# Kernel optimization log

Hardware: AMD Instinct MI355X
Metric: run time of the kernel (lower is better)

Reference implementation:

```python
import jax, jax.numpy as jnp
import numpy as np

N = 50000
NEG_SLOPE_ATT = 0.2    # PyG GATConv attention leaky_relu slope
NEG_SLOPE_ACT = 0.01   # torch F.leaky_relu default slope


def leaky(x, s):
    return jnp.where(x >= 0, x, s * x)


def gat_conv(x, src, dst, W, att_src, att_dst, bias):
    """PyG GATConv (concat=True, dropout off, self-loops already in src/dst).
    x: [N, F_in]; W: [F_in, H*C]; att_src/att_dst: [H, C]; bias: [H*C]."""
    H, C = att_src.shape
    h = (x @ W).reshape(N, H, C)                       # [N, H, C]
    a_src = (h * att_src[None]).sum(-1)                # [N, H]
    a_dst = (h * att_dst[None]).sum(-1)                # [N, H]
    e = leaky(a_src[src] + a_dst[dst], NEG_SLOPE_ATT)  # [E, H]
    # numerically-stable softmax over incoming edges of each dst node
    m = jax.ops.segment_max(e, dst, num_segments=N)    # [N, H]
    ex = jnp.exp(e - m[dst])
    Z = jax.ops.segment_sum(ex, dst, num_segments=N)   # [N, H]
    alpha = ex / (Z[dst] + 1e-16)                      # [E, H]
    msg = h[src] * alpha[:, :, None]                   # [E, H, C]
    out = jax.ops.segment_sum(msg, dst, num_segments=N)
    return out.reshape(N, H * C) + bias[None, :]


def setup_inputs() -> dict:
    key = jax.random.key(0)
    ks = jax.random.split(key, 12)
    E = 800000
    in_c, hid, heads, out_c = 256, 32, 4, 128
    hc = hid * heads  # 128
    x = jax.random.normal(ks[0], (N, in_c), dtype=jnp.float32)
    edge_index = jax.random.randint(ks[1], (2, E), 0, N, dtype=jnp.int64)
    s1 = 1.0 / np.sqrt(in_c)
    s2 = 1.0 / np.sqrt(hc)
    return {
        "x": x,
        "edge_index": edge_index,
        "W1": jax.random.normal(ks[2], (in_c, heads * hid), dtype=jnp.float32) * s1,
        "att_src1": jax.random.normal(ks[3], (heads, hid), dtype=jnp.float32) * s2,
        "att_dst1": jax.random.normal(ks[4], (heads, hid), dtype=jnp.float32) * s2,
        "b1": jnp.zeros((hc,), dtype=jnp.float32),
        "W2": jax.random.normal(ks[5], (hc, out_c), dtype=jnp.float32) * s2,
        "att_src2": jax.random.normal(ks[6], (1, out_c), dtype=jnp.float32) * s2,
        "att_dst2": jax.random.normal(ks[7], (1, out_c), dtype=jnp.float32) * s2,
        "b2": jnp.zeros((out_c,), dtype=jnp.float32),
    }


def reference(x, edge_index, W1, att_src1, att_dst1, b1, W2, att_src2, att_dst2, b2):
    # add self loops (PyG GATConv default add_self_loops=True)
    loops = jnp.arange(N, dtype=edge_index.dtype)
    src = jnp.concatenate([edge_index[0], loops])
    dst = jnp.concatenate([edge_index[1], loops])
    h = leaky(gat_conv(x, src, dst, W1, att_src1, att_dst1, b1), NEG_SLOPE_ACT)
    out = leaky(gat_conv(h, src, dst, W2, att_src2, att_dst2, b2), NEG_SLOPE_ACT)
    return out
```

## Files before the change

kernel.cpp:

```cpp
#include <hip/hip_runtime.h>
#include <hip/hip_fp16.h>

#define SLOPE_ATT 0.2f
#define SLOPE_ACT 0.01f

#define NB_CSR 128
#define CHUNK 8192

typedef _Float16 hf8 __attribute__((ext_vector_type(8)));
typedef float f32x4 __attribute__((ext_vector_type(4)));

template<int K, int H, bool A_FP32>
__device__ __forceinline__
void gemm_mfma_body(int gbid, int tid,
                    const void* __restrict__ Av, const _Float16* __restrict__ BT,
                    const float* __restrict__ att_s, const float* __restrict__ att_d,
                    _Float16* __restrict__ hout, float* __restrict__ a_src,
                    float* __restrict__ a_dst, int M)
{
  const int lane = tid & 63;
  const int wid  = tid >> 6;
  const int li   = lane & 15;
  const int lk   = lane >> 4;
  const int rowbase = gbid * 128 + wid * 32;

  const float*    Af = (const float*)Av;
  const _Float16* Ah = (const _Float16*)Av;

  f32x4 acc[2][8];
#pragma unroll
  for (int i = 0; i < 2; ++i)
#pragma unroll
    for (int j = 0; j < 8; ++j) acc[i][j] = (f32x4){0.f, 0.f, 0.f, 0.f};

  const int r0 = min(rowbase + li,      M - 1);
  const int r1 = min(rowbase + 16 + li, M - 1);

#pragma unroll
  for (int ks = 0; ks < K / 32; ++ks) {
    const int kb = ks * 32 + lk * 8;
    hf8 a0, a1;
    if constexpr (A_FP32) {
      const float* p0 = &Af[(size_t)r0 * K + kb];
      const float* p1 = &Af[(size_t)r1 * K + kb];
      float4 x0a = *(const float4*)p0, x0b = *(const float4*)(p0 + 4);
      float4 x1a = *(const float4*)p1, x1b = *(const float4*)(p1 + 4);
      a0[0]=(_Float16)x0a.x; a0[1]=(_Float16)x0a.y; a0[2]=(_Float16)x0a.z; a0[3]=(_Float16)x0a.w;
      a0[4]=(_Float16)x0b.x; a0[5]=(_Float16)x0b.y; a0[6]=(_Float16)x0b.z; a0[7]=(_Float16)x0b.w;
      a1[0]=(_Float16)x1a.x; a1[1]=(_Float16)x1a.y; a1[2]=(_Float16)x1a.z; a1[3]=(_Float16)x1a.w;
      a1[4]=(_Float16)x1b.x; a1[5]=(_Float16)x1b.y; a1[6]=(_Float16)x1b.z; a1[7]=(_Float16)x1b.w;
    } else {
      a0 = *(const hf8*)&Ah[(size_t)r0 * K + kb];
      a1 = *(const hf8*)&Ah[(size_t)r1 * K + kb];
    }
#pragma unroll
    for (int cf = 0; cf < 8; ++cf) {
      hf8 b = *(const hf8*)&BT[(size_t)(cf * 16 + li) * K + kb];
      acc[0][cf] = __builtin_amdgcn_mfma_f32_16x16x32_f16(a0, b, acc[0][cf], 0, 0, 0);
      acc[1][cf] = __builtin_amdgcn_mfma_f32_16x16x32_f16(a1, b, acc[1][cf], 0, 0, 0);
    }
  }

  float sA[8], dA[8];
#pragma unroll
  for (int cf = 0; cf < 8; ++cf) {
    sA[cf] = att_s[cf * 16 + li];
    dA[cf] = att_d[cf * 16 + li];
  }

  const bool full = (rowbase + 32) <= M;
#pragma unroll
  for (int rf = 0; rf < 2; ++rf) {
    const int rb = rowbase + rf * 16 + lk * 4;
#pragma unroll
    for (int reg = 0; reg < 4; ++reg) {
      const int r = rb + reg;
      if (full || r < M) {
#pragma unroll
        for (int cf = 0; cf < 8; ++cf)
          hout[(size_t)r * 128 + cf * 16 + li] = (_Float16)acc[rf][cf][reg];
      }
    }
    if constexpr (H == 4) {
#pragma unroll
      for (int hh = 0; hh < 4; ++hh) {
#pragma unroll
        for (int reg = 0; reg < 4; ++reg) {
          float sp = acc[rf][2*hh][reg] * sA[2*hh] + acc[rf][2*hh+1][reg] * sA[2*hh+1];
          float dp = acc[rf][2*hh][reg] * dA[2*hh] + acc[rf][2*hh+1][reg] * dA[2*hh+1];
          sp += __shfl_xor(sp, 1); sp += __shfl_xor(sp, 2);
          sp += __shfl_xor(sp, 4); sp += __shfl_xor(sp, 8);
          dp += __shfl_xor(dp, 1); dp += __shfl_xor(dp, 2);
          dp += __shfl_xor(dp, 4); dp += __shfl_xor(dp, 8);
          const int r = rb + reg;
          if (li == 0 && r < M) {
            a_src[(size_t)r * 4 + hh] = sp;
            a_dst[(size_t)r * 4 + hh] = dp;
          }
        }
      }
    } else {
#pragma unroll
      for (int reg = 0; reg < 4; ++reg) {
        float sp = 0.f, dp = 0.f;
#pragma unroll
        for (int cf = 0; cf < 8; ++cf) {
          sp += acc[rf][cf][reg] * sA[cf];
          dp += acc[rf][cf][reg] * dA[cf];
        }
        sp += __shfl_xor(sp, 1); sp += __shfl_xor(sp, 2);
        sp += __shfl_xor(sp, 4); sp += __shfl_xor(sp, 8);
        dp += __shfl_xor(dp, 1); dp += __shfl_xor(dp, 2);
        dp += __shfl_xor(dp, 4); dp += __shfl_xor(dp, 8);
        const int r = rb + reg;
        if (li == 0 && r < M) { a_src[r] = sp; a_dst[r] = dp; }
      }
    }
  }
}

__global__ __launch_bounds__(256)
void fused_pre_kernel(const int* __restrict__ ei, int E, int N,
                      unsigned short* __restrict__ cnt16mat,
                      unsigned short* __restrict__ rank16,
                      unsigned* __restrict__ sd32,
                      const float* __restrict__ W1, _Float16* __restrict__ W1T,
                      const float* __restrict__ W2, _Float16* __restrict__ W2T,
                      int ncount)
{
  __shared__ unsigned cnt[CHUNK];
  const int bid = blockIdx.x;
  if (bid < ncount) {
    const int b = bid % NB_CSR;
    const int c0 = (bid / NB_CSR) * CHUNK;
    const int clen = min(CHUNK, N - c0);
    const int EE = E + N;
    const int epb = (EE + NB_CSR - 1) / NB_CSR;
    const int lo = b * epb, hi = min(lo + epb, EE);

    for (int j = threadIdx.x; j < clen; j += 256) cnt[j] = 0;
    __syncthreads();
    for (int i = lo + threadIdx.x; i < hi; i += 256) {
      int d = (i < E) ? ei[E + i] : (i - E);
      int r = d - c0;
      if (r >= 0 && r < clen) {
        unsigned rank = atomicAdd(&cnt[r], 1u);
        rank16[i] = (unsigned short)rank;
      }
    }
    __syncthreads();
    for (int j = threadIdx.x; j < clen; j += 256)
      cnt16mat[(size_t)b * N + c0 + j] = (unsigned short)cnt[j];
  } else {
    int rem = bid - ncount;
    if (rem < 128) {
      int idx = rem * 256 + threadIdx.x;
      int k = idx >> 7, c = idx & 127;
      W1T[(size_t)c * 256 + k] = (_Float16)W1[idx];
    } else if (rem < 192) {
      int idx = (rem - 128) * 256 + threadIdx.x;
      int k = idx >> 7, c = idx & 127;
      W2T[(size_t)c * 128 + k] = (_Float16)W2[idx];
    } else {
      const int i = (rem - 192) * 256 + threadIdx.x;
      const int EE = E + N;
      if (i < EE) {
        unsigned s, d;
        if (i < E) { s = (unsigned)ei[i]; d = (unsigned)ei[E + i]; }
        else       { s = d = (unsigned)(i - E); }
        sd32[i] = (s << 16) | d;
      }
    }
  }
}

__global__ __launch_bounds__(256)
void colscan_kernel(unsigned short* __restrict__ cnt16mat,
                    unsigned* __restrict__ deg, unsigned* __restrict__ bsum, int N)
{
  __shared__ unsigned red[256];
  const int d2 = blockIdx.x * 256 + threadIdx.x;
  const int N2 = N >> 1;
  unsigned off0 = 0, off1 = 0;
  if (d2 < N2) {
    unsigned* pm = (unsigned*)cnt16mat;
#pragma unroll 8
    for (int b = 0; b < NB_CSR; ++b) {
      unsigned t = pm[(size_t)b * N2 + d2];
      pm[(size_t)b * N2 + d2] = off0 | (off1 << 16);
      off0 += t & 0xFFFFu;
      off1 += t >> 16;
    }
    deg[2 * d2]     = off0;
    deg[2 * d2 + 1] = off1;
  }
  red[threadIdx.x] = off0 + off1;
  __syncthreads();
  for (int o = 128; o; o >>= 1) {
    if (threadIdx.x < o) red[threadIdx.x] += red[threadIdx.x + o];
    __syncthreads();
  }
  if (threadIdx.x == 0) bsum[blockIdx.x] = red[0];
}

__global__ __launch_bounds__(256)
void rowstart_kernel(const unsigned* __restrict__ deg, const unsigned* __restrict__ bsum,
                     unsigned* __restrict__ row_start, int N, int nblk)
{
  __shared__ unsigned s[256];
  __shared__ unsigned boff_sh;
  const int t = threadIdx.x;
  unsigned v0 = (t < nblk) ? bsum[t] : 0u;
  s[t] = v0;
  __syncthreads();
  for (int off = 1; off < 256; off <<= 1) {
    unsigned v = (t >= off) ? s[t - off] : 0u;
    __syncthreads();
    s[t] += v;
    __syncthreads();
  }
  if (t == (int)blockIdx.x) boff_sh = s[t] - v0;
  __syncthreads();
  const unsigned boff = boff_sh;
  __syncthreads();
  const int i = blockIdx.x * 512 + t * 2;
  unsigned d0 = (i < N) ? deg[i] : 0u;
  unsigned d1 = (i + 1 < N) ? deg[i + 1] : 0u;
  s[t] = d0 + d1;
  __syncthreads();
  for (int off = 1; off < 256; off <<= 1) {
    unsigned v = (t >= off) ? s[t - off] : 0u;
    __syncthreads();
    s[t] += v;
    __syncthreads();
  }
  unsigned base = boff + s[t] - (d0 + d1);
  if (i < N)     row_start[i] = base;
  if (i + 1 < N) row_start[i + 1] = base + d0;
}

__global__ __launch_bounds__(256)
void fused_mid_kernel(int E, int N, int epb,
                      const unsigned* __restrict__ sd32,
                      const unsigned short* __restrict__ cnt16mat,
                      const unsigned short* __restrict__ rank16,
                      const unsigned* __restrict__ row_start,
                      unsigned short* __restrict__ csr16,
                      const float* __restrict__ x, const _Float16* __restrict__ W1T,
                      const float* __restrict__ as1, const float* __restrict__ ad1,
                      _Float16* __restrict__ h, float* __restrict__ asv,
                      float* __restrict__ adv, int ggrid)
{
  const int bid = blockIdx.x;
  if (bid < ggrid) {
    gemm_mfma_body<256, 4, true>(bid, threadIdx.x, x, W1T, as1, ad1,
                                 h, asv, adv, N);
  } else {
    const int i = (bid - ggrid) * 256 + threadIdx.x;
    const int EE = E + N;
    if (i < EE) {
      const unsigned sd = sd32[i];
      const unsigned d = sd & 0xFFFFu;
      const int b = i / epb;
      unsigned pos = row_start[d] + cnt16mat[(size_t)b * N + d] + rank16[i];
      csr16[pos] = (unsigned short)(sd >> 16);
    }
  }
}

__global__ __launch_bounds__(256)
void agg1_gemm2_kernel(const unsigned* __restrict__ row_start,
                       const unsigned* __restrict__ deg,
                       const unsigned short* __restrict__ csr16,
                       const __half* __restrict__ h,
                       const float* __restrict__ a_src,
                       const float* __restrict__ a_dst,
                       const float* __restrict__ bias,
                       const _Float16* __restrict__ W2T,
                       const float* __restrict__ as2, const float* __restrict__ ad2,
                       _Float16* __restrict__ h2,
                       float* __restrict__ asv2, float* __restrict__ adv2, int N)
{
  __shared__ _Float16 actS[16][136];
  __shared__ float sdots[2][16];

  const int lane = threadIdx.x & 63;
  const int wid  = threadIdx.x >> 6;
  const int l5   = lane & 15;
  const int nl   = wid * 4 + (lane >> 4);
  const int nb   = blockIdx.x * 16;
  const int n    = nb + nl;
  const int nn   = min(n, N - 1);
  const int hd   = l5 >> 2;

  const float adn = a_dst[(size_t)nn * 4 + hd];
  const unsigned beg = row_start[nn];
  const unsigned cnt = deg[nn];
  unsigned cmax = cnt;
  cmax = max(cmax, (unsigned)__shfl_xor((int)cmax, 16));
  cmax = max(cmax, (unsigned)__shfl_xor((int)cmax, 32));

  const float4* __restrict__ h4 = (const float4*)h;

  float Z = 0.f;
  float acc[8];
#pragma unroll
  for (int j = 0; j < 8; ++j) acc[j] = 0.f;

  unsigned i = 0;
  for (; i + 2 <= cmax; i += 2) {
    unsigned s0 = csr16[beg + min(i,     cnt - 1)];
    unsigned s1 = csr16[beg + min(i + 1, cnt - 1)];
    float e0 = a_src[(size_t)s0 * 4 + hd] + adn;
    float e1 = a_src[(size_t)s1 * 4 + hd] + adn;
    float4 v0 = h4[(size_t)s0 * 16 + l5];
    float4 v1 = h4[(size_t)s1 * 16 + l5];
    e0 = (e0 >= 0.f) ? e0 : SLOPE_ATT * e0;
    e1 = (e1 >= 0.f) ? e1 : SLOPE_ATT * e1;
    float w0 = (i     < cnt) ? __expf(e0) : 0.f;
    float w1 = (i + 1 < cnt) ? __expf(e1) : 0.f;
    Z += w0 + w1;
    const __half2* p0 = (const __half2*)&v0;
    const __half2* p1 = (const __half2*)&v1;
#pragma unroll
    for (int j = 0; j < 4; ++j) {
      float2 f0 = __half22float2(p0[j]);
      float2 f1 = __half22float2(p1[j]);
      acc[2*j]   += w0 * f0.x + w1 * f1.x;
      acc[2*j+1] += w0 * f0.y + w1 * f1.y;
    }
  }
  if (i < cmax) {
    unsigned s0 = csr16[beg + min(i, cnt - 1)];
    float e0 = a_src[(size_t)s0 * 4 + hd] + adn;
    float4 v0 = h4[(size_t)s0 * 16 + l5];
    e0 = (e0 >= 0.f) ? e0 : SLOPE_ATT * e0;
    float w0 = (i < cnt) ? __expf(e0) : 0.f;
    Z += w0;
    const __half2* p0 = (const __half2*)&v0;
#pragma unroll
    for (int j = 0; j < 4; ++j) {
      float2 f0 = __half22float2(p0[j]);
      acc[2*j]   += w0 * f0.x;
      acc[2*j+1] += w0 * f0.y;
    }
  }

  const float inv = 1.f / (Z + 1e-16f);
  float4 b0 = ((const float4*)bias)[l5 * 2];
  float4 b1 = ((const float4*)bias)[l5 * 2 + 1];
  float o[8];
  o[0] = acc[0] * inv + b0.x;  o[1] = acc[1] * inv + b0.y;
  o[2] = acc[2] * inv + b0.z;  o[3] = acc[3] * inv + b0.w;
  o[4] = acc[4] * inv + b1.x;  o[5] = acc[5] * inv + b1.y;
  o[6] = acc[6] * inv + b1.z;  o[7] = acc[7] * inv + b1.w;
#pragma unroll
  for (int j = 0; j < 8; ++j) o[j] = (o[j] >= 0.f) ? o[j] : SLOPE_ACT * o[j];

#pragma unroll
  for (int j = 0; j < 8; ++j) actS[nl][l5 * 8 + j] = (_Float16)o[j];
  if (threadIdx.x < 32) sdots[threadIdx.x >> 4][threadIdx.x & 15] = 0.f;
  __syncthreads();

  const int li = l5;
  const int lk = lane >> 4;
#pragma unroll
  for (int t = 0; t < 2; ++t) {
    const int c0 = wid * 32 + t * 16;
    f32x4 a2 = (f32x4){0.f, 0.f, 0.f, 0.f};
#pragma unroll
    for (int ks = 0; ks < 4; ++ks) {
      hf8 af = *(const hf8*)&actS[li][ks * 32 + lk * 8];
      hf8 bf = *(const hf8*)&W2T[(size_t)(c0 + li) * 128 + ks * 32 + lk * 8];
      a2 = __builtin_amdgcn_mfma_f32_16x16x32_f16(af, bf, a2, 0, 0, 0);
    }
    const float asc = as2[c0 + li];
    const float adc = ad2[c0 + li];
#pragma unroll
    for (int reg = 0; reg < 4; ++reg) {
      const int r = lk * 4 + reg;
      float hv = a2[reg];
      if (nb + r < N) h2[(size_t)(nb + r) * 128 + c0 + li] = (_Float16)hv;
      float sp = hv * asc;
      float dp = hv * adc;
      sp += __shfl_xor(sp, 1); sp += __shfl_xor(sp, 2);
      sp += __shfl_xor(sp, 4); sp += __shfl_xor(sp, 8);
      dp += __shfl_xor(dp, 1); dp += __shfl_xor(dp, 2);
      dp += __shfl_xor(dp, 4); dp += __shfl_xor(dp, 8);
      if (li == 0) {
        atomicAdd(&sdots[0][r], sp);
        atomicAdd(&sdots[1][r], dp);
      }
    }
  }
  __syncthreads();
  if (threadIdx.x < 16) {
    const int r = threadIdx.x;
    if (nb + r < N) {
      asv2[nb + r] = sdots[0][r];
      adv2[nb + r] = sdots[1][r];
    }
  }
}

__global__ __launch_bounds__(256)
void aggregate2_kernel(const unsigned* __restrict__ row_start,
                       const unsigned* __restrict__ deg,
                       const unsigned short* __restrict__ csr16,
                       const __half* __restrict__ h,
                       const float* __restrict__ a_src,
                       const float* __restrict__ a_dst,
                       const float* __restrict__ bias,
                       float* __restrict__ out, int N)
{
  const int lane = threadIdx.x & 63;
  const int wid  = threadIdx.x >> 6;
  const int l5   = lane & 15;
  const int n    = blockIdx.x * 16 + wid * 4 + (lane >> 4);
  const int nn   = min(n, N - 1);

  const float adn = a_dst[nn];
  const unsigned beg = row_start[nn];
  const unsigned cnt = deg[nn];
  unsigned cmax = cnt;
  cmax = max(cmax, (unsigned)__shfl_xor((int)cmax, 16));
  cmax = max(cmax, (unsigned)__shfl_xor((int)cmax, 32));

  const float4* __restrict__ h4 = (const float4*)h;

  float Z = 0.f;
  float acc[8];
#pragma unroll
  for (int j = 0; j < 8; ++j) acc[j] = 0.f;

  unsigned i = 0;
  for (; i + 2 <= cmax; i += 2) {
    unsigned s0 = csr16[beg + min(i,     cnt - 1)];
    unsigned s1 = csr16[beg + min(i + 1, cnt - 1)];
    float e0 = a_src[s0] + adn;
    float e1 = a_src[s1] + adn;
    float4 v0 = h4[(size_t)s0 * 16 + l5];
    float4 v1 = h4[(size_t)s1 * 16 + l5];
    e0 = (e0 >= 0.f) ? e0 : SLOPE_ATT * e0;
    e1 = (e1 >= 0.f) ? e1 : SLOPE_ATT * e1;
    float w0 = (i     < cnt) ? __expf(e0) : 0.f;
    float w1 = (i + 1 < cnt) ? __expf(e1) : 0.f;
    Z += w0 + w1;
    const __half2* p0 = (const __half2*)&v0;
    const __half2* p1 = (const __half2*)&v1;
#pragma unroll
    for (int j = 0; j < 4; ++j) {
      float2 f0 = __half22float2(p0[j]);
      float2 f1 = __half22float2(p1[j]);
      acc[2*j]   += w0 * f0.x + w1 * f1.x;
      acc[2*j+1] += w0 * f0.y + w1 * f1.y;
    }
  }
  if (i < cmax) {
    unsigned s0 = csr16[beg + min(i, cnt - 1)];
    float e0 = a_src[s0] + adn;
    float4 v0 = h4[(size_t)s0 * 16 + l5];
    e0 = (e0 >= 0.f) ? e0 : SLOPE_ATT * e0;
    float w0 = (i < cnt) ? __expf(e0) : 0.f;
    Z += w0;
    const __half2* p0 = (const __half2*)&v0;
#pragma unroll
    for (int j = 0; j < 4; ++j) {
      float2 f0 = __half22float2(p0[j]);
      acc[2*j]   += w0 * f0.x;
      acc[2*j+1] += w0 * f0.y;
    }
  }

  const float inv = 1.f / (Z + 1e-16f);
  float4 b0 = ((const float4*)bias)[l5 * 2];
  float4 b1 = ((const float4*)bias)[l5 * 2 + 1];
  float o[8];
  o[0] = acc[0] * inv + b0.x;  o[1] = acc[1] * inv + b0.y;
  o[2] = acc[2] * inv + b0.z;  o[3] = acc[3] * inv + b0.w;
  o[4] = acc[4] * inv + b1.x;  o[5] = acc[5] * inv + b1.y;
  o[6] = acc[6] * inv + b1.z;  o[7] = acc[7] * inv + b1.w;
#pragma unroll
  for (int j = 0; j < 8; ++j) o[j] = (o[j] >= 0.f) ? o[j] : SLOPE_ACT * o[j];

  if (n < N) {
    ((float4*)out)[(size_t)n * 32 + l5 * 2]     = make_float4(o[0], o[1], o[2], o[3]);
    ((float4*)out)[(size_t)n * 32 + l5 * 2 + 1] = make_float4(o[4], o[5], o[6], o[7]);
  }
}

extern "C" void kernel_launch(void* const* d_in, const int* in_sizes, int n_in,
                              void* d_out, int out_size, void* d_ws, size_t ws_size,
                              hipStream_t stream)
{
  const float* x   = (const float*)d_in[0];
  const int*   ei  = (const int*)d_in[1];
  const float* W1  = (const float*)d_in[2];
  const float* as1 = (const float*)d_in[3];
  const float* ad1 = (const float*)d_in[4];
  const float* b1  = (const float*)d_in[5];
  const float* W2  = (const float*)d_in[6];
  const float* as2 = (const float*)d_in[7];
  const float* ad2 = (const float*)d_in[8];
  const float* b2  = (const float*)d_in[9];
  float* out = (float*)d_out;

  const int N  = in_sizes[0] / 256;
  const int E  = in_sizes[1] / 2;
  const int EE = E + N;
  const int NCH  = (N + CHUNK - 1) / CHUNK;
  const int nblk = (N + 511) / 512;
  const int NSC  = NB_CSR * NCH;
  const int epb  = (EE + NB_CSR - 1) / NB_CSR;
  const int pgrid = (EE + 255) / 256;

  float* ws = (float*)d_ws;
  size_t o = 0;
  _Float16* h    = (_Float16*)(ws + o); o += (size_t)N * 64;
  _Float16* h2   = (_Float16*)(ws + o); o += (size_t)N * 64;
  float* asv  = ws + o; o += (size_t)N * 4;
  float* adv  = ws + o; o += (size_t)N * 4;
  float* asv2 = ws + o; o += (size_t)N;
  float* adv2 = ws + o; o += (size_t)N;
  _Float16* W1T = (_Float16*)(ws + o); o += 128 * 256 / 2;
  _Float16* W2T = (_Float16*)(ws + o); o += 128 * 128 / 2;
  unsigned* deg       = (unsigned*)(ws + o); o += (size_t)N;
  unsigned* row_start = (unsigned*)(ws + o); o += (size_t)N;
  unsigned* bsum      = (unsigned*)(ws + o); o += 256;
  unsigned* sd32      = (unsigned*)(ws + o); o += (size_t)EE;
  unsigned short* csr16    = (unsigned short*)(ws + o); o += (size_t)(EE + 1) / 2;
  unsigned short* cnt16mat = (unsigned short*)(ws + o); o += (size_t)NB_CSR * N / 2;
  unsigned short* rank16   = (unsigned short*)(ws + o); o += (size_t)(EE + 1) / 2;

  const int ngrid = (N + 15) / 16;
  const int ggrid = (N + 127) / 128;
  const int sgrid = (EE + 255) / 256;

  fused_pre_kernel<<<NSC + 192 + pgrid, 256, 0, stream>>>(
      ei, E, N, cnt16mat, rank16, sd32, W1, W1T, W2, W2T, NSC);
  colscan_kernel<<<nblk, 256, 0, stream>>>(cnt16mat, deg, bsum, N);
  rowstart_kernel<<<nblk, 256, 0, stream>>>(deg, bsum, row_start, N, nblk);
  fused_mid_kernel<<<ggrid + sgrid, 256, 0, stream>>>(
      E, N, epb, sd32, cnt16mat, rank16, row_start, csr16,
      x, W1T, as1, ad1, h, asv, adv, ggrid);
  agg1_gemm2_kernel<<<ngrid, 256, 0, stream>>>(
      row_start, deg, csr16, (const __half*)h, asv, adv, b1,
      W2T, as2, ad2, h2, asv2, adv2, N);
  aggregate2_kernel<<<ngrid, 256, 0, stream>>>(
      row_start, deg, csr16, (const __half*)h2, asv2, adv2, b2, out, N);
}
```

Before: 168.7 us.

## Replace per-node count matrix CSR build with two-level bucket radix sort

Replaces the CSR construction, which used a 128×N 16-bit count matrix, a column scan and a row-start scan, with a two-pass bucket sort. Edges are first histogrammed into 128-node buckets per block, then scanned per bucket and scattered into bucket order. Each bucket is then sorted locally in shared memory to produce deg, row_start and csr16. This drops the large count-matrix traffic and the rank array, but edge order within a row is no longer deterministic because of shared-memory atomics. It also adds an extra scatter pass and repeats the bucket-start scan in every block. The aggregation kernel's shared-memory padding is also changed from 136 to 132.

```diff
diff --git a/kernel.cpp b/kernel.cpp
--- a/kernel.cpp
+++ b/kernel.cpp
@@ -4,8 +4,8 @@
 #define SLOPE_ATT 0.2f
 #define SLOPE_ACT 0.01f
 
-#define NB_CSR 128
-#define CHUNK 8192
+#define SB 256
+#define NBUKMAX 512
 
 typedef _Float16 hf8 __attribute__((ext_vector_type(8)));
 typedef float f32x4 __attribute__((ext_vector_type(4)));
@@ -120,97 +120,54 @@
 }
 
 __global__ __launch_bounds__(256)
-void fused_pre_kernel(const int* __restrict__ ei, int E, int N,
-                      unsigned short* __restrict__ cnt16mat,
-                      unsigned short* __restrict__ rank16,
-                      unsigned* __restrict__ sd32,
-                      const float* __restrict__ W1, _Float16* __restrict__ W1T,
-                      const float* __restrict__ W2, _Float16* __restrict__ W2T,
-                      int ncount)
-{
-  __shared__ unsigned cnt[CHUNK];
+void pre_kernel(const int* __restrict__ ei, int E, int N, int nbuk, int epb1,
+                unsigned* __restrict__ cntA, unsigned* __restrict__ sd32,
+                const float* __restrict__ W1, _Float16* __restrict__ W1T,
+                const float* __restrict__ W2, _Float16* __restrict__ W2T)
+{
+  __shared__ unsigned hist[NBUKMAX];
   const int bid = blockIdx.x;
-  if (bid < ncount) {
-    const int b = bid % NB_CSR;
-    const int c0 = (bid / NB_CSR) * CHUNK;
-    const int clen = min(CHUNK, N - c0);
+  const int tid = threadIdx.x;
+  if (bid < SB) {
+    for (int j = tid; j < NBUKMAX; j += 256) hist[j] = 0;
+    __syncthreads();
     const int EE = E + N;
-    const int epb = (EE + NB_CSR - 1) / NB_CSR;
-    const int lo = b * epb, hi = min(lo + epb, EE);
-
-    for (int j = threadIdx.x; j < clen; j += 256) cnt[j] = 0;
-    __syncthreads();
-    for (int i = lo + threadIdx.x; i < hi; i += 256) {
+    const int lo = bid * epb1, hi = min(lo + epb1, EE);
+    for (int i = lo + tid; i < hi; i += 256) {
       int d = (i < E) ? ei[E + i] : (i - E);
-      int r = d - c0;
-      if (r >= 0 && r < clen) {
-        unsigned rank = atomicAdd(&cnt[r], 1u);
-        rank16[i] = (unsigned short)rank;
-      }
-    }
-    __syncthreads();
-    for (int j = threadIdx.x; j < clen; j += 256)
-      cnt16mat[(size_t)b * N + c0 + j] = (unsigned short)cnt[j];
+      atomicAdd(&hist[d >> 7], 1u);
+    }
+    __syncthreads();
+    for (int j = tid; j < nbuk; j += 256)
+      cntA[(size_t)bid * NBUKMAX + j] = hist[j];
+  } else if (bid < SB + 128) {
+    int idx = (bid - SB) * 256 + tid;
+    int k = idx >> 7, c = idx & 127;
+    W1T[(size_t)c * 256 + k] = (_Float16)W1[idx];
+  } else if (bid < SB + 192) {
+    int idx = (bid - SB - 128) * 256 + tid;
+    int k = idx >> 7, c = idx & 127;
+    W2T[(size_t)c * 128 + k] = (_Float16)W2[idx];
   } else {
-    int rem = bid - ncount;
-    if (rem < 128) {
-      int idx = rem * 256 + threadIdx.x;
-      int k = idx >> 7, c = idx & 127;
-      W1T[(size_t)c * 256 + k] = (_Float16)W1[idx];
-    } else if (rem < 192) {
-      int idx = (rem - 128) * 256 + threadIdx.x;
-      int k = idx >> 7, c = idx & 127;
-      W2T[(size_t)c * 128 + k] = (_Float16)W2[idx];
-    } else {
-      const int i = (rem - 192) * 256 + threadIdx.x;
-      const int EE = E + N;
-      if (i < EE) {
-        unsigned s, d;
-        if (i < E) { s = (unsigned)ei[i]; d = (unsigned)ei[E + i]; }
-        else       { s = d = (unsigned)(i - E); }
-        sd32[i] = (s << 16) | d;
-      }
+    const int i = (bid - SB - 192) * 256 + tid;
+    const int EE = E + N;
+    if (i < EE) {
+      unsigned s, d;
+      if (i < E) { s = (unsigned)ei[i]; d = (unsigned)ei[E + i]; }
+      else       { s = d = (unsigned)(i - E); }
+      sd32[i] = (s << 16) | d;
     }
   }
 }
 
 __global__ __launch_bounds__(256)
-void colscan_kernel(unsigned short* __restrict__ cnt16mat,
-                    unsigned* __restrict__ deg, unsigned* __restrict__ bsum, int N)
-{
-  __shared__ unsigned red[256];
-  const int d2 = blockIdx.x * 256 + threadIdx.x;
-  const int N2 = N >> 1;
-  unsigned off0 = 0, off1 = 0;
-  if (d2 < N2) {
-    unsigned* pm = (unsigned*)cnt16mat;
-#pragma unroll 8
-    for (int b = 0; b < NB_CSR; ++b) {
-      unsigned t = pm[(size_t)b * N2 + d2];
-      pm[(size_t)b * N2 + d2] = off0 | (off1 << 16);
-      off0 += t & 0xFFFFu;
-      off1 += t >> 16;
-    }
-    deg[2 * d2]     = off0;
-    deg[2 * d2 + 1] = off1;
-  }
-  red[threadIdx.x] = off0 + off1;
-  __syncthreads();
-  for (int o = 128; o; o >>= 1) {
-    if (threadIdx.x < o) red[threadIdx.x] += red[threadIdx.x + o];
-    __syncthreads();
-  }
-  if (threadIdx.x == 0) bsum[blockIdx.x] = red[0];
-}
-
-__global__ __launch_bounds__(256)
-void rowstart_kernel(const unsigned* __restrict__ deg, const unsigned* __restrict__ bsum,
-                     unsigned* __restrict__ row_start, int N, int nblk)
+void bukoff_kernel(const unsigned* __restrict__ cntA, unsigned* __restrict__ blkoff,
+                   unsigned* __restrict__ buktotal)
 {
   __shared__ unsigned s[256];
-  __shared__ unsigned boff_sh;
+  const int j = blockIdx.x;
   const int t = threadIdx.x;
-  unsigned v0 = (t < nblk) ? bsum[t] : 0u;
+  unsigned v0 = cntA[(size_t)t * NBUKMAX + j];
   s[t] = v0;
   __syncthreads();
   for (int off = 1; off < 256; off <<= 1) {
@@ -219,52 +176,111 @@
     s[t] += v;
     __syncthreads();
   }
-  if (t == (int)blockIdx.x) boff_sh = s[t] - v0;
-  __syncthreads();
-  const unsigned boff = boff_sh;
-  __syncthreads();
-  const int i = blockIdx.x * 512 + t * 2;
-  unsigned d0 = (i < N) ? deg[i] : 0u;
-  unsigned d1 = (i + 1 < N) ? deg[i + 1] : 0u;
-  s[t] = d0 + d1;
+  blkoff[(size_t)t * NBUKMAX + j] = s[t] - v0;
+  if (t == 255) buktotal[j] = s[255];
+}
+
+__device__ __forceinline__
+void bukstart_scan(const unsigned* __restrict__ buktotal, int nbuk,
+                   unsigned* bt, unsigned* ps, unsigned* bs, int tid)
+{
+  for (int j = tid; j < NBUKMAX; j += 256) bt[j] = (j < nbuk) ? buktotal[j] : 0u;
+  __syncthreads();
+  unsigned pair = bt[2 * tid] + bt[2 * tid + 1];
+  ps[tid] = pair;
   __syncthreads();
   for (int off = 1; off < 256; off <<= 1) {
-    unsigned v = (t >= off) ? s[t - off] : 0u;
-    __syncthreads();
-    s[t] += v;
-    __syncthreads();
-  }
-  unsigned base = boff + s[t] - (d0 + d1);
-  if (i < N)     row_start[i] = base;
-  if (i + 1 < N) row_start[i + 1] = base + d0;
+    unsigned v = (tid >= off) ? ps[tid - off] : 0u;
+    __syncthreads();
+    ps[tid] += v;
+    __syncthreads();
+  }
+  unsigned e0 = ps[tid] - pair;
+  bs[2 * tid]     = e0;
+  bs[2 * tid + 1] = e0 + bt[2 * tid];
+  __syncthreads();
 }
 
 __global__ __launch_bounds__(256)
-void fused_mid_kernel(int E, int N, int epb,
-                      const unsigned* __restrict__ sd32,
-                      const unsigned short* __restrict__ cnt16mat,
-                      const unsigned short* __restrict__ rank16,
-                      const unsigned* __restrict__ row_start,
-                      unsigned short* __restrict__ csr16,
-                      const float* __restrict__ x, const _Float16* __restrict__ W1T,
-                      const float* __restrict__ as1, const float* __restrict__ ad1,
-                      _Float16* __restrict__ h, float* __restrict__ asv,
-                      float* __restrict__ adv, int ggrid)
-{
+void gemm1_scatter_kernel(int E, int N, int nbuk, int epb1,
+                          const unsigned* __restrict__ sd32,
+                          const unsigned* __restrict__ blkoff,
+                          const unsigned* __restrict__ buktotal,
+                          unsigned* __restrict__ ebuk,
+                          const float* __restrict__ x, const _Float16* __restrict__ W1T,
+                          const float* __restrict__ as1, const float* __restrict__ ad1,
+                          _Float16* __restrict__ h, float* __restrict__ asv,
+                          float* __restrict__ adv, int ggrid)
+{
+  __shared__ unsigned bt[NBUKMAX], bs[NBUKMAX], cur[NBUKMAX];
+  __shared__ unsigned ps[256];
   const int bid = blockIdx.x;
+  const int tid = threadIdx.x;
   if (bid < ggrid) {
-    gemm_mfma_body<256, 4, true>(bid, threadIdx.x, x, W1T, as1, ad1,
-                                 h, asv, adv, N);
+    gemm_mfma_body<256, 4, true>(bid, tid, x, W1T, as1, ad1, h, asv, adv, N);
   } else {
-    const int i = (bid - ggrid) * 256 + threadIdx.x;
+    const int sb = bid - ggrid;
+    bukstart_scan(buktotal, nbuk, bt, ps, bs, tid);
+    for (int j = tid; j < nbuk; j += 256)
+      cur[j] = bs[j] + blkoff[(size_t)sb * NBUKMAX + j];
+    __syncthreads();
     const int EE = E + N;
-    if (i < EE) {
-      const unsigned sd = sd32[i];
-      const unsigned d = sd & 0xFFFFu;
-      const int b = i / epb;
-      unsigned pos = row_start[d] + cnt16mat[(size_t)b * N + d] + rank16[i];
-      csr16[pos] = (unsigned short)(sd >> 16);
-    }
+    const int lo = sb * epb1, hi = min(lo + epb1, EE);
+    for (int i = lo + tid; i < hi; i += 256) {
+      unsigned sd = sd32[i];
+      unsigned buk = (sd & 0xFFFFu) >> 7;
+      unsigned slot = atomicAdd(&cur[buk], 1u);
+      ebuk[slot] = sd;
+    }
+  }
+}
+
+__global__ __launch_bounds__(256)
+void csr_build_kernel(int N, int nbuk,
+                      const unsigned* __restrict__ buktotal,
+                      const unsigned* __restrict__ ebuk,
+                      unsigned* __restrict__ deg, unsigned* __restrict__ row_start,
+                      unsigned short* __restrict__ csr16)
+{
+  __shared__ unsigned bt[NBUKMAX], bs[NBUKMAX];
+  __shared__ unsigned ps[256];
+  __shared__ unsigned hist[128], hs[128], cur2[128];
+  const int j = blockIdx.x;
+  const int tid = threadIdx.x;
+
+  bukstart_scan(buktotal, nbuk, bt, ps, bs, tid);
+  const unsigned estart = bs[j];
+  const unsigned ecount = bt[j];
+  const int n0 = j * 128;
+
+  if (tid < 128) hist[tid] = 0;
+  __syncthreads();
+  for (unsigned i = estart + tid; i < estart + ecount; i += 256)
+    atomicAdd(&hist[ebuk[i] & 127u], 1u);
+  __syncthreads();
+  unsigned hv = (tid < 128) ? hist[tid] : 0u;
+  if (tid < 128) hs[tid] = hv;
+  __syncthreads();
+  for (int off = 1; off < 128; off <<= 1) {
+    unsigned v = 0;
+    if (tid < 128 && tid >= off) v = hs[tid - off];
+    __syncthreads();
+    if (tid < 128) hs[tid] += v;
+    __syncthreads();
+  }
+  if (tid < 128) {
+    unsigned excl = hs[tid] - hv;
+    cur2[tid] = estart + excl;
+    if (n0 + tid < N) {
+      deg[n0 + tid] = hv;
+      row_start[n0 + tid] = estart + excl;
+    }
+  }
+  __syncthreads();
+  for (unsigned i = estart + tid; i < estart + ecount; i += 256) {
+    unsigned sd = ebuk[i];
+    unsigned slot = atomicAdd(&cur2[sd & 127u], 1u);
+    csr16[slot] = (unsigned short)(sd >> 16);
   }
 }
 
@@ -281,7 +297,7 @@
                        _Float16* __restrict__ h2,
                        float* __restrict__ asv2, float* __restrict__ adv2, int N)
 {
-  __shared__ _Float16 actS[16][136];
+  __shared__ _Float16 actS[16][132];
   __shared__ float sdots[2][16];
 
   const int lane = threadIdx.x & 63;
@@ -508,10 +524,8 @@
   const int N  = in_sizes[0] / 256;
   const int E  = in_sizes[1] / 2;
   const int EE = E + N;
-  const int NCH  = (N + CHUNK - 1) / CHUNK;
-  const int nblk = (N + 511) / 512;
-  const int NSC  = NB_CSR * NCH;
-  const int epb  = (EE + NB_CSR - 1) / NB_CSR;
+  const int nbuk = (N + 127) / 128;
+  const int epb1 = (EE + SB - 1) / SB;
   const int pgrid = (EE + 255) / 256;
 
   float* ws = (float*)d_ws;
@@ -526,23 +540,24 @@
   _Float16* W2T = (_Float16*)(ws + o); o += 128 * 128 / 2;
   unsigned* deg       = (unsigned*)(ws + o); o += (size_t)N;
   unsigned* row_start = (unsigned*)(ws + o); o += (size_t)N;
-  unsigned* bsum      = (unsigned*)(ws + o); o += 256;
+  unsigned* cntA      = (unsigned*)(ws + o); o += (size_t)SB * NBUKMAX;
+  unsigned* blkoff    = (unsigned*)(ws + o); o += (size_t)SB * NBUKMAX;
+  unsigned* buktotal  = (unsigned*)(ws + o); o += NBUKMAX;
   unsigned* sd32      = (unsigned*)(ws + o); o += (size_t)EE;
-  unsigned short* csr16    = (unsigned short*)(ws + o); o += (size_t)(EE + 1) / 2;
-  unsigned short* cnt16mat = (unsigned short*)(ws + o); o += (size_t)NB_CSR * N / 2;
-  unsigned short* rank16   = (unsigned short*)(ws + o); o += (size_t)(EE + 1) / 2;
+  unsigned* ebuk      = (unsigned*)(ws + o); o += (size_t)EE;
+  unsigned short* csr16 = (unsigned short*)(ws + o); o += (size_t)(EE + 1) / 2;
 
   const int ngrid = (N + 15) / 16;
   const int ggrid = (N + 127) / 128;
-  const int sgrid = (EE + 255) / 256;
-
-  fused_pre_kernel<<<NSC + 192 + pgrid, 256, 0, stream>>>(
-      ei, E, N, cnt16mat, rank16, sd32, W1, W1T, W2, W2T, NSC);
-  colscan_kernel<<<nblk, 256, 0, stream>>>(cnt16mat, deg, bsum, N);
-  rowstart_kernel<<<nblk, 256, 0, stream>>>(deg, bsum, row_start, N, nblk);
-  fused_mid_kernel<<<ggrid + sgrid, 256, 0, stream>>>(
-      E, N, epb, sd32, cnt16mat, rank16, row_start, csr16,
+
+  pre_kernel<<<SB + 192 + pgrid, 256, 0, stream>>>(
+      ei, E, N, nbuk, epb1, cntA, sd32, W1, W1T, W2, W2T);
+  bukoff_kernel<<<nbuk, 256, 0, stream>>>(cntA, blkoff, buktotal);
+  gemm1_scatter_kernel<<<ggrid + SB, 256, 0, stream>>>(
+      E, N, nbuk, epb1, sd32, blkoff, buktotal, ebuk,
       x, W1T, as1, ad1, h, asv, adv, ggrid);
+  csr_build_kernel<<<nbuk, 256, 0, stream>>>(
+      N, nbuk, buktotal, ebuk, deg, row_start, csr16);
   agg1_gemm2_kernel<<<ngrid, 256, 0, stream>>>(
       row_start, deg, csr16, (const __half*)h, asv, adv, b1,
       W2T, as2, ad2, h2, asv2, adv2, N);
```

Measured after the change: 144.0 us. 1.17x faster.
